# Performance work log

Measured on AMD Instinct MI355X. Metric: run time of the kernel, lower is better.

Reference implementation:

```python
import jax, jax.numpy as jnp
import numpy as np

PATCH_SIZE = 2  # init arg patch_size


def setup_inputs() -> dict:
    key = jax.random.key(0)
    k1, k2, k3, k4, k5 = jax.random.split(key, 5)
    b, H, W, d = 8, 32, 32, 256
    n_obj = 15
    patches = jax.random.normal(k1, (b, H, W, d), jnp.float32)
    embs = jax.random.normal(k2, (b, n_obj, 256), jnp.float32)
    locations = jax.random.randint(k3, (b, n_obj, 4), 0, 32, jnp.int32)
    Wp = jax.random.normal(k4, (256, 256), jnp.float32) * 0.05
    We = jax.random.normal(k5, (256, 256), jnp.float32) * 0.05
    return {"patches": patches, "embs": embs, "locations": locations, "Wp": Wp, "We": We}


def _build_masks(locations, b, H, W):
    # patching(): floor starts / ceil ends to multiples of PATCH_SIZE
    starts = locations[..., :2] - locations[..., :2] % PATCH_SIZE
    ends = locations[..., 2:] + (PATCH_SIZE - locations[..., 2:] % PATCH_SIZE)
    locs = jnp.concatenate([starts, ends], axis=-1)          # [b, n_obj, 4]
    img = jnp.broadcast_to(jnp.array([0, 0, H, W], locs.dtype), (b, 1, 4))
    locs = jnp.concatenate([locs, img], axis=1)              # [b, n, 4]
    rows = jnp.arange(H)[:, None]                             # [H,1]
    cols = jnp.arange(W)[None, :]                             # [1,W]
    y0 = locs[..., 0, None, None]; x0 = locs[..., 1, None, None]
    y1 = locs[..., 2, None, None]; x1 = locs[..., 3, None, None]
    # vectorized box rasterization (replaces torch slice-assign scatter loops)
    m = (rows >= y0) & (rows < y1) & (cols >= x0) & (cols < x1)  # [b,n,H,W]
    return m.reshape(b, locs.shape[1], H * W)                 # [b,n,HW]


def reference(patches, embs, locations, Wp, We):
    b, H, W, d = patches.shape
    # append mean embedding (torch: cat([embs, embs.mean(dim=1, keepdim=True)]))
    embs = jnp.concatenate([embs, embs.mean(axis=1, keepdims=True)], axis=1)  # [b,n,e]
    masks = _build_masks(locations, b, H, W)                  # [b,n,HW] bool
    mf = masks.astype(patches.dtype)
    # InjectionBlock (assumed minimal): project patches, inject masked emb
    proj = jnp.einsum('bpd,do->bpo', patches.reshape(b, H * W, d), Wp)  # [b,HW,o]
    inj = jnp.einsum('bne,eo->bno', embs, We)                 # [b,n,o]
    p = proj[:, None] + mf[..., None] * inj[:, :, None, :]    # [b,n,HW,o]
    # masked mean pooling over the n mask channels
    out = (p * mf[..., None]).sum(axis=1) / mf.sum(axis=1)[..., None]  # [b,HW,o]
    return out
```

## Files before the change

kernel.cpp:

```cpp
#include <hip/hip_runtime.h>
#include <hip/hip_bf16.h>

typedef short short8 __attribute__((ext_vector_type(8)));
typedef float f32x4 __attribute__((ext_vector_type(4)));

static __device__ __forceinline__ ushort2 pk2(float a, float b) {
    __hip_bfloat162 h = __float22bfloat162_rn(make_float2(a, b));
    ushort2 r;
    __builtin_memcpy(&r, &h, 4);
    return r;
}
static __device__ __forceinline__ unsigned short bf1(float a) {
    __hip_bfloat16 h = __float2bfloat16(a);
    unsigned short r;
    __builtin_memcpy(&r, &h, 2);
    return r;
}

__global__ __launch_bounds__(256)
void fused_all(const float* __restrict__ patches,
               const float* __restrict__ embs,
               const int* __restrict__ locations,
               const float* __restrict__ Wp,
               const float* __restrict__ We,
               float* __restrict__ out) {
    __shared__ __align__(16) unsigned short Ash[64 * 256];
    __shared__ __align__(16) unsigned short Ebf[16 * 256];
    __shared__ __align__(16) unsigned short injW[4 * 16 * 32];
    __shared__ unsigned maskL[64];
    __shared__ float rcL[64];

    const int bid = blockIdx.x, t = threadIdx.x;
    const int b = bid >> 6, pt = (bid >> 2) & 15, ct = bid & 3;
    const int p0 = pt * 64, c0 = ct * 64;
    const int wv = t >> 6, lane = t & 63, lhi = lane >> 4, llo = lane & 15;
    const int oc = c0 + wv * 16 + llo;

    const float* pbase = patches + (size_t)(b * 1024 + p0) * 256;
    #pragma unroll
    for (int it = 0; it < 16; ++it) {
        int u = t + it * 256;
        int row = u >> 6, c4 = u & 63;
        float4 f = *reinterpret_cast<const float4*>(pbase + row * 256 + c4 * 4);
        ushort2 lo = pk2(f.x, f.y), hi = pk2(f.z, f.w);
        ushort4 o = {lo.x, lo.y, hi.x, hi.y};
        int byte = row * 512 + ((c4 * 8) ^ ((row & 7) << 4));
        *reinterpret_cast<ushort4*>(reinterpret_cast<char*>(Ash) + byte) = o;
    }

    if (t < 128) {
        const int c0e = t * 2;
        float s0 = 0.f, s1 = 0.f;
        #pragma unroll
        for (int r = 0; r < 15; ++r) {
            float2 v = *reinterpret_cast<const float2*>(embs + (size_t)(b * 15 + r) * 256 + c0e);
            s0 += v.x; s1 += v.y;
            ushort2 p2 = pk2(v.x, v.y);
            unsigned pk = (unsigned)p2.x | ((unsigned)p2.y << 16);
            *reinterpret_cast<unsigned*>(reinterpret_cast<char*>(Ebf)
                + r * 512 + ((c0e * 2) ^ ((r & 7) << 4))) = pk;
        }
        ushort2 p2 = pk2(s0 * (1.0f / 15.0f), s1 * (1.0f / 15.0f));
        unsigned pk = (unsigned)p2.x | ((unsigned)p2.y << 16);
        *reinterpret_cast<unsigned*>(reinterpret_cast<char*>(Ebf)
            + 15 * 512 + ((c0e * 2) ^ (7 << 4))) = pk;
    }

    if (t < 64) {
        int p = p0 + t;
        int h = p >> 5, w = p & 31;
        const int* loc = locations + b * 60;
        unsigned m = 1u << 15;
        #pragma unroll
        for (int nb = 0; nb < 15; ++nb) {
            int y0 = loc[nb * 4 + 0] & ~1;
            int x0 = loc[nb * 4 + 1] & ~1;
            int y1 = (loc[nb * 4 + 2] & ~1) + 2;
            int x1 = (loc[nb * 4 + 3] & ~1) + 2;
            if (h >= y0 && h < y1 && w >= x0 && w < x1) m |= 1u << nb;
        }
        maskL[t] = m;
        rcL[t] = 1.0f / (float)__popc(m);
    }
    __syncthreads();

    f32x4 accI = (f32x4){0.f, 0.f, 0.f, 0.f};
    #pragma unroll
    for (int ks = 0; ks < 8; ++ks) {
        const short8 afr = *reinterpret_cast<const short8*>(
            reinterpret_cast<const char*>(Ebf)
            + llo * 512 + ((ks * 64 + lhi * 16) ^ ((llo & 7) << 4)));
        short8 bfr;
        #pragma unroll
        for (int rr = 0; rr < 4; ++rr) {
            float w0 = We[(size_t)(ks * 32 + lhi * 8 + 2 * rr + 0) * 256 + oc];
            float w1 = We[(size_t)(ks * 32 + lhi * 8 + 2 * rr + 1) * 256 + oc];
            ushort2 p2 = pk2(w0, w1);
            bfr[2 * rr + 0] = (short)p2.x;
            bfr[2 * rr + 1] = (short)p2.y;
        }
        accI = __builtin_amdgcn_mfma_f32_16x16x32_bf16(afr, bfr, accI, 0, 0, 0);
    }
    {
        ushort2 lo = pk2(accI[0], accI[1]), hi = pk2(accI[2], accI[3]);
        ushort4 o4 = {lo.x, lo.y, hi.x, hi.y};
        unsigned short* dst = injW + wv * 512 + llo * 32;
        *reinterpret_cast<ushort4*>(dst + lhi * 4) = o4;
        ushort4 z = {0, 0, 0, 0};
        *reinterpret_cast<ushort4*>(dst + 16 + lhi * 4) = z;
    }
    asm volatile("s_waitcnt lgkmcnt(0)" ::: "memory");
    __builtin_amdgcn_sched_barrier(0);
    const short8 jf = *reinterpret_cast<const short8*>(injW + wv * 512 + llo * 32 + lhi * 8);

    f32x4 acc[4];
    #pragma unroll
    for (int mt = 0; mt < 4; ++mt) acc[mt] = (f32x4){0.f, 0.f, 0.f, 0.f};
    #pragma unroll
    for (int ks = 0; ks < 8; ++ks) {
        short8 bfr;
        #pragma unroll
        for (int rr = 0; rr < 4; ++rr) {
            float w0 = Wp[(size_t)(ks * 32 + lhi * 8 + 2 * rr + 0) * 256 + oc];
            float w1 = Wp[(size_t)(ks * 32 + lhi * 8 + 2 * rr + 1) * 256 + oc];
            ushort2 p2 = pk2(w0, w1);
            bfr[2 * rr + 0] = (short)p2.x;
            bfr[2 * rr + 1] = (short)p2.y;
        }
        #pragma unroll
        for (int mt = 0; mt < 4; ++mt) {
            int row = mt * 16 + llo;
            const short8 af = *reinterpret_cast<const short8*>(
                reinterpret_cast<const char*>(Ash)
                + row * 512 + (((ks * 32 + lhi * 8) * 2) ^ ((row & 7) << 4)));
            acc[mt] = __builtin_amdgcn_mfma_f32_16x16x32_bf16(af, bfr, acc[mt], 0, 0, 0);
        }
    }

    #pragma unroll
    for (int mt = 0; mt < 4; ++mt) {
        unsigned m = maskL[mt * 16 + llo];
        unsigned short rcb = bf1(rcL[mt * 16 + llo]);
        short8 mfrag;
        #pragma unroll
        for (int r = 0; r < 8; ++r) {
            int k = lhi * 8 + r;
            mfrag[r] = (k < 16 && ((m >> k) & 1u)) ? (short)rcb : (short)0;
        }
        f32x4 accE = __builtin_amdgcn_mfma_f32_16x16x32_bf16(
            mfrag, jf, (f32x4){0.f, 0.f, 0.f, 0.f}, 0, 0, 0);
        float* ob = out + (size_t)(b * 1024 + p0 + mt * 16) * 256;
        #pragma unroll
        for (int j = 0; j < 4; ++j)
            ob[(lhi * 4 + j) * 256 + oc] = acc[mt][j] + accE[j];
    }
}

extern "C" void kernel_launch(void* const* d_in, const int* in_sizes, int n_in,
                              void* d_out, int out_size, void* d_ws, size_t ws_size,
                              hipStream_t stream) {
    const float* patches = (const float*)d_in[0];
    const float* embs    = (const float*)d_in[1];
    const int*   locs    = (const int*)d_in[2];
    const float* Wp      = (const float*)d_in[3];
    const float* We      = (const float*)d_in[4];
    float* out = (float*)d_out;

    fused_all<<<512, 256, 0, stream>>>(patches, embs, locs, Wp, We, out);
}
```

Measured before the change: 16.30 us.

## Split K dimension across two wave groups with shared-memory reduction

Doubles the block size to 512 threads so each output tile's projection GEMM is split along K across two groups of four waves. Partial accumulators are exchanged through a new shared buffer and summed, and each group writes half of the output rows. The injection GEMM is computed only by the first group, and the second group reads its result after the barrier. This adds a barrier and LDS traffic but doubles the waves per block and halves each wave's serial MFMA chain, aiming to hide Wp load latency.

```diff
diff --git a/kernel.cpp b/kernel.cpp
--- a/kernel.cpp
+++ b/kernel.cpp
@@ -17,7 +17,7 @@
     return r;
 }
 
-__global__ __launch_bounds__(256)
+__global__ __launch_bounds__(512)
 void fused_all(const float* __restrict__ patches,
                const float* __restrict__ embs,
                const int* __restrict__ locations,
@@ -27,19 +27,21 @@
     __shared__ __align__(16) unsigned short Ash[64 * 256];
     __shared__ __align__(16) unsigned short Ebf[16 * 256];
     __shared__ __align__(16) unsigned short injW[4 * 16 * 32];
+    __shared__ __align__(16) float Qbuf[2 * 4 * 64 * 8];
     __shared__ unsigned maskL[64];
     __shared__ float rcL[64];
 
     const int bid = blockIdx.x, t = threadIdx.x;
     const int b = bid >> 6, pt = (bid >> 2) & 15, ct = bid & 3;
     const int p0 = pt * 64, c0 = ct * 64;
-    const int wv = t >> 6, lane = t & 63, lhi = lane >> 4, llo = lane & 15;
-    const int oc = c0 + wv * 16 + llo;
+    const int w = t >> 6, wh = w >> 2, wl = w & 3;
+    const int lane = t & 63, lhi = lane >> 4, llo = lane & 15;
+    const int oc = c0 + wl * 16 + llo;
 
     const float* pbase = patches + (size_t)(b * 1024 + p0) * 256;
     #pragma unroll
-    for (int it = 0; it < 16; ++it) {
-        int u = t + it * 256;
+    for (int it = 0; it < 8; ++it) {
+        int u = t + it * 512;
         int row = u >> 6, c4 = u & 63;
         float4 f = *reinterpret_cast<const float4*>(pbase + row * 256 + c4 * 4);
         ushort2 lo = pk2(f.x, f.y), hi = pk2(f.z, f.w);
@@ -68,7 +70,7 @@
 
     if (t < 64) {
         int p = p0 + t;
-        int h = p >> 5, w = p & 31;
+        int h = p >> 5, wpx = p & 31;
         const int* loc = locations + b * 60;
         unsigned m = 1u << 15;
         #pragma unroll
@@ -77,47 +79,50 @@
             int x0 = loc[nb * 4 + 1] & ~1;
             int y1 = (loc[nb * 4 + 2] & ~1) + 2;
             int x1 = (loc[nb * 4 + 3] & ~1) + 2;
-            if (h >= y0 && h < y1 && w >= x0 && w < x1) m |= 1u << nb;
+            if (h >= y0 && h < y1 && wpx >= x0 && wpx < x1) m |= 1u << nb;
         }
         maskL[t] = m;
         rcL[t] = 1.0f / (float)__popc(m);
     }
     __syncthreads();
 
-    f32x4 accI = (f32x4){0.f, 0.f, 0.f, 0.f};
+    short8 jf;
+    f32x4 acc[4];
     #pragma unroll
-    for (int ks = 0; ks < 8; ++ks) {
-        const short8 afr = *reinterpret_cast<const short8*>(
-            reinterpret_cast<const char*>(Ebf)
-            + llo * 512 + ((ks * 64 + lhi * 16) ^ ((llo & 7) << 4)));
-        short8 bfr;
+    for (int mt = 0; mt < 4; ++mt) acc[mt] = (f32x4){0.f, 0.f, 0.f, 0.f};
+
+    if (wh == 0) {
+        f32x4 accI = (f32x4){0.f, 0.f, 0.f, 0.f};
         #pragma unroll
-        for (int rr = 0; rr < 4; ++rr) {
-            float w0 = We[(size_t)(ks * 32 + lhi * 8 + 2 * rr + 0) * 256 + oc];
-            float w1 = We[(size_t)(ks * 32 + lhi * 8 + 2 * rr + 1) * 256 + oc];
-            ushort2 p2 = pk2(w0, w1);
-            bfr[2 * rr + 0] = (short)p2.x;
-            bfr[2 * rr + 1] = (short)p2.y;
+        for (int ks = 0; ks < 8; ++ks) {
+            const short8 afr = *reinterpret_cast<const short8*>(
+                reinterpret_cast<const char*>(Ebf)
+                + llo * 512 + ((ks * 64 + lhi * 16) ^ ((llo & 7) << 4)));
+            short8 bfr;
+            #pragma unroll
+            for (int rr = 0; rr < 4; ++rr) {
+                float w0 = We[(size_t)(ks * 32 + lhi * 8 + 2 * rr + 0) * 256 + oc];
+                float w1 = We[(size_t)(ks * 32 + lhi * 8 + 2 * rr + 1) * 256 + oc];
+                ushort2 p2 = pk2(w0, w1);
+                bfr[2 * rr + 0] = (short)p2.x;
+                bfr[2 * rr + 1] = (short)p2.y;
+            }
+            accI = __builtin_amdgcn_mfma_f32_16x16x32_bf16(afr, bfr, accI, 0, 0, 0);
         }
-        accI = __builtin_amdgcn_mfma_f32_16x16x32_bf16(afr, bfr, accI, 0, 0, 0);
-    }
-    {
         ushort2 lo = pk2(accI[0], accI[1]), hi = pk2(accI[2], accI[3]);
         ushort4 o4 = {lo.x, lo.y, hi.x, hi.y};
-        unsigned short* dst = injW + wv * 512 + llo * 32;
+        unsigned short* dst = injW + wl * 512 + llo * 32;
         *reinterpret_cast<ushort4*>(dst + lhi * 4) = o4;
         ushort4 z = {0, 0, 0, 0};
         *reinterpret_cast<ushort4*>(dst + 16 + lhi * 4) = z;
+        asm volatile("s_waitcnt lgkmcnt(0)" ::: "memory");
+        __builtin_amdgcn_sched_barrier(0);
+        jf = *reinterpret_cast<const short8*>(injW + wl * 512 + llo * 32 + lhi * 8);
     }
-    asm volatile("s_waitcnt lgkmcnt(0)" ::: "memory");
-    __builtin_amdgcn_sched_barrier(0);
-    const short8 jf = *reinterpret_cast<const short8*>(injW + wv * 512 + llo * 32 + lhi * 8);
 
-    f32x4 acc[4];
     #pragma unroll
-    for (int mt = 0; mt < 4; ++mt) acc[mt] = (f32x4){0.f, 0.f, 0.f, 0.f};
-    #pragma unroll
-    for (int ks = 0; ks < 8; ++ks) {
+    for (int ks2 = 0; ks2 < 4; ++ks2) {
+        const int ks = wh * 4 + ks2;
         short8 bfr;
         #pragma unroll
         for (int rr = 0; rr < 4; ++rr) {
@@ -137,8 +142,24 @@
         }
     }
 
+    {
+        float* qp = Qbuf + (((wh ^ 1) * 4 + wl) * 64 + lane) * 8;
+        const int mtb = (wh == 0) ? 2 : 0;
+        *reinterpret_cast<f32x4*>(qp + 0) = acc[mtb + 0];
+        *reinterpret_cast<f32x4*>(qp + 4) = acc[mtb + 1];
+    }
+    __syncthreads();
+
+    if (wh == 1)
+        jf = *reinterpret_cast<const short8*>(injW + wl * 512 + llo * 32 + lhi * 8);
+
+    const float* qr = Qbuf + ((wh * 4 + wl) * 64 + lane) * 8;
+    const int mtbase = wh * 2;
     #pragma unroll
-    for (int mt = 0; mt < 4; ++mt) {
+    for (int i = 0; i < 2; ++i) {
+        const int mt = mtbase + i;
+        f32x4 part = *reinterpret_cast<const f32x4*>(qr + i * 4);
+        f32x4 tot = acc[mt] + part;
         unsigned m = maskL[mt * 16 + llo];
         unsigned short rcb = bf1(rcL[mt * 16 + llo]);
         short8 mfrag;
@@ -152,7 +173,7 @@
         float* ob = out + (size_t)(b * 1024 + p0 + mt * 16) * 256;
         #pragma unroll
         for (int j = 0; j < 4; ++j)
-            ob[(lhi * 4 + j) * 256 + oc] = acc[mt][j] + accE[j];
+            ob[(lhi * 4 + j) * 256 + oc] = tot[j] + accE[j];
     }
 }
 
@@ -166,5 +187,5 @@
     const float* We      = (const float*)d_in[4];
     float* out = (float*)d_out;
 
-    fused_all<<<512, 256, 0, stream>>>(patches, embs, locs, Wp, We, out);
+    fused_all<<<512, 512, 0, stream>>>(patches, embs, locs, Wp, We, out);
 }
```

New measurement: 18.60 us. 14.1% more time.
